# Optimization experiments

Hardware: AMD Instinct MI355X
Metric: run time of the kernel (lower is better)

Reference implementation:

```python
import jax, jax.numpy as jnp
import numpy as np

N, M, D = 256, 64, 1024


def _l2norm(x, axis=-1, eps=1e-12):
    # tf.math.l2_normalize semantics: x / sqrt(max(sum(x^2), eps))
    sq = jnp.sum(x * x, axis=axis, keepdims=True)
    return x * jax.lax.rsqrt(jnp.maximum(sq, eps))


def setup_inputs() -> dict:
    key = jax.random.key(0)
    k1, = jax.random.split(key, 1)
    inputs = jax.random.normal(k1, (N * M, D), dtype=jnp.float32)
    w = jnp.full((1,), 10.0, dtype=jnp.float32)
    b = jnp.full((1,), -5.0, dtype=jnp.float32)
    return {"inputs": inputs, "w": w, "b": b}


def reference(inputs, w, b):
    emb = inputs.reshape(N, M, D)                       # (N, M, D)
    # speaker centroids (normalized mean over utterances)
    center = _l2norm(jnp.mean(emb, axis=1))             # (N, D)
    # leave-one-out centroid per utterance: sum over M minus self (NOT divided)
    center_except = _l2norm(jnp.sum(emb, axis=1, keepdims=True) - emb)  # (N, M, D)
    # off-diagonal similarities: every utterance vs every speaker centroid
    sim_all = jnp.einsum('jmd,id->jmi', emb, center)    # (N_utt_spk j, M, N_centroid i)
    # diagonal (i == j): utterance vs its own leave-one-out centroid
    diag = jnp.sum(center_except * emb, axis=-1)        # (N, M)
    eye = jnp.eye(N, dtype=bool)[:, None, :]            # (N, 1, N)
    sim = jnp.where(eye, diag[:, :, None], sim_all)     # (N, M, N)
    sim = w * sim + b
    return sim.reshape(N * M, N)
```

## Files before the change

kernel.cpp:

```cpp
#include <hip/hip_runtime.h>

#define NSPK 256
#define MUTT 64
#define DDIM 1024
#define NROW (NSPK * MUTT)

using frag_ab = __attribute__((ext_vector_type(8))) short;
using frag_cd = __attribute__((ext_vector_type(4))) float;

static __device__ __forceinline__ unsigned short f32_to_bf16(float f) {
    unsigned int u = __float_as_uint(f);
    return (unsigned short)((u + 0x7FFFu + ((u >> 16) & 1u)) >> 16);
}
static __device__ __forceinline__ unsigned int pack2(float a, float b) {
    return (unsigned)f32_to_bf16(a) | ((unsigned)f32_to_bf16(b) << 16);
}
static __device__ __forceinline__ void gload16(const void* g, void* l) {
    __builtin_amdgcn_global_load_lds(
        (const __attribute__((address_space(1))) unsigned int*)g,
        (__attribute__((address_space(3))) unsigned int*)l, 16, 0, 0);
}


__global__ void __launch_bounds__(256) k_prep(const float* __restrict__ emb,
                                              float* __restrict__ Sp,
                                              unsigned short* __restrict__ ebf,
                                              float* __restrict__ qg) {
    const int j = blockIdx.x;
    const int h = blockIdx.y;
    const int t = threadIdx.x;
    const int lane = t & 63, wave = t >> 6;
    const size_t rowbase = (size_t)j * MUTT + (size_t)h * 16;
    const float* src = emb + rowbase * DDIM + (size_t)t * 4;
    unsigned short* edst = ebf + rowbase * DDIM + (size_t)t * 4;
    __shared__ float qws[16][4];
    float4 s = make_float4(0.f, 0.f, 0.f, 0.f);
    #pragma unroll
    for (int m = 0; m < 16; ++m) {
        float4 v = *(const float4*)(src + (size_t)m * DDIM);
        s.x += v.x; s.y += v.y; s.z += v.z; s.w += v.w;
        float qp = v.x * v.x + v.y * v.y + v.z * v.z + v.w * v.w;
        #pragma unroll
        for (int off = 32; off > 0; off >>= 1) qp += __shfl_down(qp, off, 64);
        if (lane == 0) qws[m][wave] = qp;
        *(uint2*)(edst + (size_t)m * DDIM) = make_uint2(pack2(v.x, v.y), pack2(v.z, v.w));
    }
    __syncthreads();
    if (t < 16) qg[rowbase + t] = qws[t][0] + qws[t][1] + qws[t][2] + qws[t][3];
    *(float4*)(Sp + ((size_t)h * NSPK + j) * DDIM + (size_t)t * 4) = s;
}

template <int P, int PACKED>
__global__ void k_center(const float* __restrict__ Sp, unsigned short* __restrict__ cbf,
                         float* __restrict__ normS2g, float* __restrict__ normSg) {
    const int j = blockIdx.x;
    const int t = threadIdx.x;
    float4 v = make_float4(0.f, 0.f, 0.f, 0.f);
    #pragma unroll
    for (int p = 0; p < P; ++p) {
        float4 a = *(const float4*)(Sp + ((size_t)p * NSPK + j) * DDIM + (size_t)t * 4);
        v.x += a.x; v.y += a.y; v.z += a.z; v.w += a.w;
    }
    float sq = v.x * v.x + v.y * v.y + v.z * v.z + v.w * v.w;
    #pragma unroll
    for (int off = 32; off > 0; off >>= 1) sq += __shfl_down(sq, off, 64);
    __shared__ float ws[4];
    __shared__ float sc_sh;
    const int lane = t & 63, wave = t >> 6;
    if (lane == 0) ws[wave] = sq;
    __syncthreads();
    if (t == 0) {
        float tot = ws[0] + ws[1] + ws[2] + ws[3];
        normS2g[j] = tot;
        normSg[j]  = sqrtf(tot);
        float msq = tot * (1.0f / 4096.0f);
        sc_sh = rsqrtf(fmaxf(msq, 1e-12f)) * (1.0f / 64.0f);
    }
    __syncthreads();
    const float sc = sc_sh;
    uint2 pk = make_uint2(pack2(v.x * sc, v.y * sc), pack2(v.z * sc, v.w * sc));
    if (PACKED) {
        unsigned short* dst = cbf + (((size_t)(t >> 1) * 256 + j) * 8 + (size_t)(t & 1) * 4);
        *(uint2*)dst = pk;
    } else {
        *(uint2*)(cbf + (size_t)j * DDIM + (size_t)t * 4) = pk;
    }
}

__global__ void __launch_bounds__(256, 4)
k_gemm8(const unsigned short* __restrict__ ebf, const unsigned short* __restrict__ cbfp,
        const float* __restrict__ qg, const float* __restrict__ n2g,
        const float* __restrict__ n1g,
        const float* __restrict__ wp, const float* __restrict__ bp,
        float* __restrict__ out) {
    __shared__ unsigned short As[16 * DDIM];

    const int tid = threadIdx.x, lane = tid & 63, wave = tid >> 6;
    const int row0 = blockIdx.x * 16;
    const int quad = lane >> 4;
    const int m16 = lane & 15;

    {
        const char* ag = (const char*)(ebf + (size_t)row0 * DDIM);
        char* Ab = (char*)As;
        #pragma unroll
        for (int r = 0; r < 8; ++r) {
            const int c = r * 256 + tid;
            const int rw = c >> 7;
            const int p = c & 127;
            gload16(ag + rw * 2048 + ((p ^ (rw & 7)) << 4), Ab + rw * 2048 + (p << 4));
        }
    }

    const char* bq[4];
    #pragma unroll
    for (int cc = 0; cc < 4; ++cc)
        bq[cc] = (const char*)cbfp + ((size_t)quad * 256 + (wave * 64 + cc * 16 + m16)) * 16;

    frag_cd acc[4];
    #pragma unroll
    for (int cc = 0; cc < 4; ++cc) acc[cc] = (frag_cd){0.f, 0.f, 0.f, 0.f};

    __syncthreads();

    const char* Ar = (const char*)As + m16 * 2048;
    const int asw = m16 & 7;
    #pragma unroll 2
    for (int ks = 0; ks < 32; ++ks) {
        frag_ab af = *(const frag_ab*)(Ar + ((((ks << 2) + quad) ^ asw) << 4));
        frag_ab bf0 = *(const frag_ab*)(bq[0] + (size_t)ks * 16384);
        frag_ab bf1 = *(const frag_ab*)(bq[1] + (size_t)ks * 16384);
        frag_ab bf2 = *(const frag_ab*)(bq[2] + (size_t)ks * 16384);
        frag_ab bf3 = *(const frag_ab*)(bq[3] + (size_t)ks * 16384);
        acc[0] = __builtin_amdgcn_mfma_f32_16x16x32_bf16(af, bf0, acc[0], 0, 0, 0);
        acc[1] = __builtin_amdgcn_mfma_f32_16x16x32_bf16(af, bf1, acc[1], 0, 0, 0);
        acc[2] = __builtin_amdgcn_mfma_f32_16x16x32_bf16(af, bf2, acc[2], 0, 0, 0);
        acc[3] = __builtin_amdgcn_mfma_f32_16x16x32_bf16(af, bf3, acc[3], 0, 0, 0);
    }

    const float wv = wp[0], bv = bp[0];
    const int jspk = row0 >> 6;
    const float ns2 = n2g[jspk], ns = n1g[jspk];
    const int rbase = quad << 2;
    #pragma unroll
    for (int cc = 0; cc < 4; ++cc) {
        int col = wave * 64 + cc * 16 + m16;
        frag_cd v = acc[cc];
        #pragma unroll
        for (int r2 = 0; r2 < 4; ++r2) {
            int grow = row0 + rbase + r2;
            float val = v[r2];
            if (col == jspk) {
                float q = qg[grow];
                float rd = val * ns;
                float den2 = ns2 - 2.f * rd + q;
                val = (rd - q) * rsqrtf(fmaxf(den2, 1e-12f));
            }
            out[(size_t)grow * NSPK + col] = wv * val + bv;
        }
    }
}


__global__ void k_sums(const float* __restrict__ emb, float* __restrict__ Sp) {
    const int j = blockIdx.x;
    const int h = blockIdx.y;
    const int c = threadIdx.x;
    const float* base = emb + ((size_t)j * MUTT + (size_t)h * 32) * DDIM + (size_t)c * 4;
    float4 acc = make_float4(0.f, 0.f, 0.f, 0.f);
    #pragma unroll 8
    for (int m = 0; m < 32; ++m) {
        float4 v = *(const float4*)(base + (size_t)m * DDIM);
        acc.x += v.x; acc.y += v.y; acc.z += v.z; acc.w += v.w;
    }
    *(float4*)(Sp + ((size_t)h * NSPK + j) * DDIM + (size_t)c * 4) = acc;
}

__global__ void __launch_bounds__(256)
k_gemm_old(const float* __restrict__ emb, const unsigned short* __restrict__ cbf,
           const float* __restrict__ normS2g, const float* __restrict__ normSg,
           const float* __restrict__ wp, const float* __restrict__ bp,
           float* __restrict__ out) {
    __shared__ unsigned short Asm[32][32];
    __shared__ unsigned short Bsm[256][32];
    __shared__ float qpart[32][8];
    __shared__ float qfin[32];
    const int tid = threadIdx.x, lane = tid & 63, wave = tid >> 6;
    const int row0 = blockIdx.x * 32;
    const int jspk = row0 >> 6;
    frag_cd acc[2][4];
    #pragma unroll
    for (int rr = 0; rr < 2; ++rr)
        #pragma unroll
        for (int cc = 0; cc < 4; ++cc) acc[rr][cc] = (frag_cd){0.f, 0.f, 0.f, 0.f};
    const int ar = tid >> 3, ak = (tid & 7) << 2;
    const float* aptr = emb + (size_t)(row0 + ar) * DDIM + ak;
    float qacc = 0.f;
    const int bi = tid >> 2, bk = (tid & 3) << 3;
    const int am = lane & 15, kq = (lane >> 4) << 3;
    for (int k0 = 0; k0 < DDIM; k0 += 32) {
        __syncthreads();
        float4 av = *(const float4*)(aptr + k0);
        qacc += av.x * av.x + av.y * av.y + av.z * av.z + av.w * av.w;
        *(uint2*)&Asm[ar][ak] = make_uint2(pack2(av.x, av.y), pack2(av.z, av.w));
        #pragma unroll
        for (int p = 0; p < 4; ++p) {
            int brow = p * 64 + bi;
            *(uint4*)&Bsm[brow][bk] = *(const uint4*)(cbf + (size_t)brow * DDIM + k0 + bk);
        }
        __syncthreads();
        frag_ab afr[2], bfr[4];
        #pragma unroll
        for (int rr = 0; rr < 2; ++rr) afr[rr] = *(const frag_ab*)&Asm[rr * 16 + am][kq];
        #pragma unroll
        for (int cc = 0; cc < 4; ++cc) bfr[cc] = *(const frag_ab*)&Bsm[wave * 64 + cc * 16 + am][kq];
        #pragma unroll
        for (int rr = 0; rr < 2; ++rr)
            #pragma unroll
            for (int cc = 0; cc < 4; ++cc)
                acc[rr][cc] = __builtin_amdgcn_mfma_f32_16x16x32_bf16(afr[rr], bfr[cc], acc[rr][cc], 0, 0, 0);
    }
    qpart[ar][tid & 7] = qacc;
    __syncthreads();
    if (tid < 32) {
        float s = 0.f;
        #pragma unroll
        for (int u = 0; u < 8; ++u) s += qpart[tid][u];
        qfin[tid] = s;
    }
    __syncthreads();
    const float wv = wp[0], bv = bp[0];
    const float ns2 = normS2g[jspk], ns = normSg[jspk];
    #pragma unroll
    for (int rr = 0; rr < 2; ++rr) {
        int rbase = rr * 16 + ((lane >> 4) << 2);
        #pragma unroll
        for (int cc = 0; cc < 4; ++cc) {
            int col = wave * 64 + cc * 16 + (lane & 15);
            frag_cd v = acc[rr][cc];
            #pragma unroll
            for (int r2 = 0; r2 < 4; ++r2) {
                int lrow = rbase + r2;
                float val = v[r2];
                if (col == jspk) {
                    float q = qfin[lrow];
                    float rd = val * ns;
                    float den2 = ns2 - 2.f * rd + q;
                    val = (rd - q) * rsqrtf(fmaxf(den2, 1e-12f));
                }
                out[(size_t)(row0 + lrow) * NSPK + col] = wv * val + bv;
            }
        }
    }
}

extern "C" void kernel_launch(void* const* d_in, const int* in_sizes, int n_in,
                              void* d_out, int out_size, void* d_ws, size_t ws_size,
                              hipStream_t stream) {
    const float* emb = (const float*)d_in[0];
    const float* w   = (const float*)d_in[1];
    const float* b   = (const float*)d_in[2];
    float* out = (float*)d_out;

    const size_t sz_Sp  = (size_t)4 * NSPK * DDIM * 4;
    const size_t sz_ebf = (size_t)NROW * DDIM * 2;
    const size_t sz_cbf = (size_t)NSPK * DDIM * 2;
    const size_t sz_qg  = (size_t)NROW * 4;
    const size_t need = sz_Sp + sz_ebf + sz_cbf + sz_qg + 2 * NSPK * 4;

    if (ws_size >= need) {
        char* p = (char*)d_ws;
        float* Sp = (float*)p;              p += sz_Sp;
        unsigned short* ebf = (unsigned short*)p; p += sz_ebf;
        unsigned short* cbf = (unsigned short*)p; p += sz_cbf;
        float* qg = (float*)p;              p += sz_qg;
        float* n2 = (float*)p;              p += NSPK * 4;
        float* n1 = n2 + NSPK;
        k_prep<<<dim3(NSPK, 4), 256, 0, stream>>>(emb, Sp, ebf, qg);
        k_center<4, 1><<<NSPK, 256, 0, stream>>>(Sp, cbf, n2, n1);
        k_gemm8<<<NROW / 16, 256, 0, stream>>>(ebf, cbf, qg, n2, n1, w, b, out);
    } else {
        float* Sp = (float*)d_ws;
        unsigned short* cbf = (unsigned short*)(Sp + 2 * NSPK * DDIM);
        float* n2 = (float*)(cbf + NSPK * DDIM);
        float* n1 = n2 + NSPK;
        k_sums<<<dim3(NSPK, 2), 256, 0, stream>>>(emb, Sp);
        k_center<2, 0><<<NSPK, 256, 0, stream>>>(Sp, cbf, n2, n1);
        k_gemm_old<<<NROW / 32, 256, 0, stream>>>(emb, cbf, n2, n1, w, b, out);
    }
}
```

Baseline: 137.1 us.

## Use 32-row GEMM tiles and compute row norms with MFMA self-products

The GEMM kernel now handles 32 rows per block, so each centroid B fragment loaded from global memory is reused across two A row tiles. The per-row squared norms are no longer written by the prep kernel. They are computed inside the GEMM with extra MFMA self-products on the bf16 A fragments, whose diagonal is read back through shared memory. The prep kernel drops its shuffle reductions and shared-memory sync, uses wider 16-byte stores, and writes 8 partial-sum slices, so the center kernel now reduces 8 partials. In exchange, q is now taken from bf16-rounded values, and the larger LDS footprint lowers occupancy to 2 blocks per SIMD bound.

```diff
diff --git a/kernel.cpp b/kernel.cpp
--- a/kernel.cpp
+++ b/kernel.cpp
@@ -24,30 +24,30 @@
 
 __global__ void __launch_bounds__(256) k_prep(const float* __restrict__ emb,
                                               float* __restrict__ Sp,
-                                              unsigned short* __restrict__ ebf,
-                                              float* __restrict__ qg) {
+                                              unsigned short* __restrict__ ebf) {
     const int j = blockIdx.x;
     const int h = blockIdx.y;
     const int t = threadIdx.x;
-    const int lane = t & 63, wave = t >> 6;
-    const size_t rowbase = (size_t)j * MUTT + (size_t)h * 16;
-    const float* src = emb + rowbase * DDIM + (size_t)t * 4;
-    unsigned short* edst = ebf + rowbase * DDIM + (size_t)t * 4;
-    __shared__ float qws[16][4];
-    float4 s = make_float4(0.f, 0.f, 0.f, 0.f);
-    #pragma unroll
-    for (int m = 0; m < 16; ++m) {
-        float4 v = *(const float4*)(src + (size_t)m * DDIM);
-        s.x += v.x; s.y += v.y; s.z += v.z; s.w += v.w;
-        float qp = v.x * v.x + v.y * v.y + v.z * v.z + v.w * v.w;
-        #pragma unroll
-        for (int off = 32; off > 0; off >>= 1) qp += __shfl_down(qp, off, 64);
-        if (lane == 0) qws[m][wave] = qp;
-        *(uint2*)(edst + (size_t)m * DDIM) = make_uint2(pack2(v.x, v.y), pack2(v.z, v.w));
-    }
-    __syncthreads();
-    if (t < 16) qg[rowbase + t] = qws[t][0] + qws[t][1] + qws[t][2] + qws[t][3];
-    *(float4*)(Sp + ((size_t)h * NSPK + j) * DDIM + (size_t)t * 4) = s;
+    const int half = t >> 7;
+    const int c8 = (t & 127) * 8;
+    const size_t rowbase = (size_t)j * MUTT + (size_t)h * 16 + (size_t)half * 8;
+    const float* src = emb + rowbase * DDIM + c8;
+    unsigned short* dst = ebf + rowbase * DDIM + c8;
+    float4 s0 = make_float4(0.f, 0.f, 0.f, 0.f);
+    float4 s1 = make_float4(0.f, 0.f, 0.f, 0.f);
+    #pragma unroll
+    for (int m = 0; m < 8; ++m) {
+        float4 a = *(const float4*)(src + (size_t)m * DDIM);
+        float4 b = *(const float4*)(src + (size_t)m * DDIM + 4);
+        s0.x += a.x; s0.y += a.y; s0.z += a.z; s0.w += a.w;
+        s1.x += b.x; s1.y += b.y; s1.z += b.z; s1.w += b.w;
+        uint4 pk = make_uint4(pack2(a.x, a.y), pack2(a.z, a.w),
+                              pack2(b.x, b.y), pack2(b.z, b.w));
+        *(uint4*)(dst + (size_t)m * DDIM) = pk;
+    }
+    float* sp = Sp + ((size_t)(h * 2 + half) * NSPK + j) * DDIM + c8;
+    *(float4*)sp = s0;
+    *(float4*)(sp + 4) = s1;
 }
 
 template <int P, int PACKED>
@@ -80,23 +80,23 @@
     const float sc = sc_sh;
     uint2 pk = make_uint2(pack2(v.x * sc, v.y * sc), pack2(v.z * sc, v.w * sc));
     if (PACKED) {
-        unsigned short* dst = cbf + (((size_t)(t >> 1) * 256 + j) * 8 + (size_t)(t & 1) * 4);
-        *(uint2*)dst = pk;
+        unsigned short* dstp = cbf + (((size_t)(t >> 1) * 256 + j) * 8 + (size_t)(t & 1) * 4);
+        *(uint2*)dstp = pk;
     } else {
         *(uint2*)(cbf + (size_t)j * DDIM + (size_t)t * 4) = pk;
     }
 }
 
-__global__ void __launch_bounds__(256, 4)
-k_gemm8(const unsigned short* __restrict__ ebf, const unsigned short* __restrict__ cbfp,
-        const float* __restrict__ qg, const float* __restrict__ n2g,
-        const float* __restrict__ n1g,
+__global__ void __launch_bounds__(256, 2)
+k_gemm9(const unsigned short* __restrict__ ebf, const unsigned short* __restrict__ cbfp,
+        const float* __restrict__ n2g, const float* __restrict__ n1g,
         const float* __restrict__ wp, const float* __restrict__ bp,
         float* __restrict__ out) {
-    __shared__ unsigned short As[16 * DDIM];
+    __shared__ unsigned short As[32 * DDIM];
+    __shared__ float qsh[32];
 
     const int tid = threadIdx.x, lane = tid & 63, wave = tid >> 6;
-    const int row0 = blockIdx.x * 16;
+    const int row0 = blockIdx.x * 32;
     const int quad = lane >> 4;
     const int m16 = lane & 15;
 
@@ -104,7 +104,7 @@
         const char* ag = (const char*)(ebf + (size_t)row0 * DDIM);
         char* Ab = (char*)As;
         #pragma unroll
-        for (int r = 0; r < 8; ++r) {
+        for (int r = 0; r < 16; ++r) {
             const int c = r * 256 + tid;
             const int rw = c >> 7;
             const int p = c & 127;
@@ -117,46 +117,71 @@
     for (int cc = 0; cc < 4; ++cc)
         bq[cc] = (const char*)cbfp + ((size_t)quad * 256 + (wave * 64 + cc * 16 + m16)) * 16;
 
-    frag_cd acc[4];
-    #pragma unroll
-    for (int cc = 0; cc < 4; ++cc) acc[cc] = (frag_cd){0.f, 0.f, 0.f, 0.f};
-
-    __syncthreads();
-
-    const char* Ar = (const char*)As + m16 * 2048;
+    frag_cd acc[2][4], accq[2];
+    #pragma unroll
+    for (int rr = 0; rr < 2; ++rr) {
+        accq[rr] = (frag_cd){0.f, 0.f, 0.f, 0.f};
+        #pragma unroll
+        for (int cc = 0; cc < 4; ++cc) acc[rr][cc] = (frag_cd){0.f, 0.f, 0.f, 0.f};
+    }
+
+    __syncthreads();
+
+    const char* Ar0 = (const char*)As + m16 * 2048;
+    const char* Ar1 = (const char*)As + (16 + m16) * 2048;
     const int asw = m16 & 7;
     #pragma unroll 2
     for (int ks = 0; ks < 32; ++ks) {
-        frag_ab af = *(const frag_ab*)(Ar + ((((ks << 2) + quad) ^ asw) << 4));
+        const int co = ((((ks << 2) + quad) ^ asw) << 4);
+        frag_ab af0 = *(const frag_ab*)(Ar0 + co);
+        frag_ab af1 = *(const frag_ab*)(Ar1 + co);
         frag_ab bf0 = *(const frag_ab*)(bq[0] + (size_t)ks * 16384);
         frag_ab bf1 = *(const frag_ab*)(bq[1] + (size_t)ks * 16384);
         frag_ab bf2 = *(const frag_ab*)(bq[2] + (size_t)ks * 16384);
         frag_ab bf3 = *(const frag_ab*)(bq[3] + (size_t)ks * 16384);
-        acc[0] = __builtin_amdgcn_mfma_f32_16x16x32_bf16(af, bf0, acc[0], 0, 0, 0);
-        acc[1] = __builtin_amdgcn_mfma_f32_16x16x32_bf16(af, bf1, acc[1], 0, 0, 0);
-        acc[2] = __builtin_amdgcn_mfma_f32_16x16x32_bf16(af, bf2, acc[2], 0, 0, 0);
-        acc[3] = __builtin_amdgcn_mfma_f32_16x16x32_bf16(af, bf3, acc[3], 0, 0, 0);
-    }
+        acc[0][0] = __builtin_amdgcn_mfma_f32_16x16x32_bf16(af0, bf0, acc[0][0], 0, 0, 0);
+        acc[0][1] = __builtin_amdgcn_mfma_f32_16x16x32_bf16(af0, bf1, acc[0][1], 0, 0, 0);
+        acc[0][2] = __builtin_amdgcn_mfma_f32_16x16x32_bf16(af0, bf2, acc[0][2], 0, 0, 0);
+        acc[0][3] = __builtin_amdgcn_mfma_f32_16x16x32_bf16(af0, bf3, acc[0][3], 0, 0, 0);
+        acc[1][0] = __builtin_amdgcn_mfma_f32_16x16x32_bf16(af1, bf0, acc[1][0], 0, 0, 0);
+        acc[1][1] = __builtin_amdgcn_mfma_f32_16x16x32_bf16(af1, bf1, acc[1][1], 0, 0, 0);
+        acc[1][2] = __builtin_amdgcn_mfma_f32_16x16x32_bf16(af1, bf2, acc[1][2], 0, 0, 0);
+        acc[1][3] = __builtin_amdgcn_mfma_f32_16x16x32_bf16(af1, bf3, acc[1][3], 0, 0, 0);
+        accq[0] = __builtin_amdgcn_mfma_f32_16x16x32_bf16(af0, af0, accq[0], 0, 0, 0);
+        accq[1] = __builtin_amdgcn_mfma_f32_16x16x32_bf16(af1, af1, accq[1], 0, 0, 0);
+    }
+
+    if (wave == 0) {
+        #pragma unroll
+        for (int rr = 0; rr < 2; ++rr)
+            #pragma unroll
+            for (int r2 = 0; r2 < 4; ++r2)
+                if (m16 == (quad << 2) + r2) qsh[rr * 16 + m16] = accq[rr][r2];
+    }
+    __syncthreads();
 
     const float wv = wp[0], bv = bp[0];
     const int jspk = row0 >> 6;
     const float ns2 = n2g[jspk], ns = n1g[jspk];
-    const int rbase = quad << 2;
-    #pragma unroll
-    for (int cc = 0; cc < 4; ++cc) {
-        int col = wave * 64 + cc * 16 + m16;
-        frag_cd v = acc[cc];
-        #pragma unroll
-        for (int r2 = 0; r2 < 4; ++r2) {
-            int grow = row0 + rbase + r2;
-            float val = v[r2];
-            if (col == jspk) {
-                float q = qg[grow];
-                float rd = val * ns;
-                float den2 = ns2 - 2.f * rd + q;
-                val = (rd - q) * rsqrtf(fmaxf(den2, 1e-12f));
+    #pragma unroll
+    for (int rr = 0; rr < 2; ++rr) {
+        const int rbase = rr * 16 + (quad << 2);
+        #pragma unroll
+        for (int cc = 0; cc < 4; ++cc) {
+            int col = wave * 64 + cc * 16 + m16;
+            frag_cd v = acc[rr][cc];
+            #pragma unroll
+            for (int r2 = 0; r2 < 4; ++r2) {
+                int lrow = rbase + r2;
+                float val = v[r2];
+                if (col == jspk) {
+                    float q = qsh[lrow];
+                    float rd = val * ns;
+                    float den2 = ns2 - 2.f * rd + q;
+                    val = (rd - q) * rsqrtf(fmaxf(den2, 1e-12f));
+                }
+                out[(size_t)(row0 + lrow) * NSPK + col] = wv * val + bv;
             }
-            out[(size_t)grow * NSPK + col] = wv * val + bv;
         }
     }
 }
@@ -262,23 +287,21 @@
     const float* b   = (const float*)d_in[2];
     float* out = (float*)d_out;
 
-    const size_t sz_Sp  = (size_t)4 * NSPK * DDIM * 4;
+    const size_t sz_Sp  = (size_t)8 * NSPK * DDIM * 4;
     const size_t sz_ebf = (size_t)NROW * DDIM * 2;
     const size_t sz_cbf = (size_t)NSPK * DDIM * 2;
-    const size_t sz_qg  = (size_t)NROW * 4;
-    const size_t need = sz_Sp + sz_ebf + sz_cbf + sz_qg + 2 * NSPK * 4;
+    const size_t need = sz_Sp + sz_ebf + sz_cbf + 2 * NSPK * 4;
 
     if (ws_size >= need) {
         char* p = (char*)d_ws;
         float* Sp = (float*)p;              p += sz_Sp;
         unsigned short* ebf = (unsigned short*)p; p += sz_ebf;
         unsigned short* cbf = (unsigned short*)p; p += sz_cbf;
-        float* qg = (float*)p;              p += sz_qg;
         float* n2 = (float*)p;              p += NSPK * 4;
-        float* n1 = n2 + NSPK;
-        k_prep<<<dim3(NSPK, 4), 256, 0, stream>>>(emb, Sp, ebf, qg);
-        k_center<4, 1><<<NSPK, 256, 0, stream>>>(Sp, cbf, n2, n1);
-        k_gemm8<<<NROW / 16, 256, 0, stream>>>(ebf, cbf, qg, n2, n1, w, b, out);
+        float* n1 = (float*)p;
+        k_prep<<<dim3(NSPK, 4), 256, 0, stream>>>(emb, Sp, ebf);
+        k_center<8, 1><<<NSPK, 256, 0, stream>>>(Sp, cbf, n2, n1);
+        k_gemm9<<<NROW / 32, 256, 0, stream>>>(ebf, cbf, n2, n1, w, b, out);
     } else {
         float* Sp = (float*)d_ws;
         unsigned short* cbf = (unsigned short*)(Sp + 2 * NSPK * DDIM);
```

Result: faster. 131.9 us (-3.8%).
